# Performance work log

Measured on AMD Instinct MI355X. Metric: run time of the kernel, lower is better.

Reference implementation:

```python
import jax, jax.numpy as jnp
import numpy as np

N_NODES = 100000
N_EDGES = 1600000
D = 128
NUM_GRAPHS = 128


def setup_inputs() -> dict:
    key = jax.random.key(0)
    ks = jax.random.split(key, 9)
    s = 1.0 / np.sqrt(D)
    return {
        "h": jax.random.normal(ks[0], (N_NODES, D), dtype=jnp.float32),
        "W1_self": jax.random.normal(ks[1], (D, D), dtype=jnp.float32) * s,
        "W1_neigh": jax.random.normal(ks[2], (D, D), dtype=jnp.float32) * s,
        "b1": jnp.zeros((D,), dtype=jnp.float32),
        "W2_self": jax.random.normal(ks[3], (D, D), dtype=jnp.float32) * s,
        "W2_neigh": jax.random.normal(ks[4], (D, D), dtype=jnp.float32) * s,
        "b2": jnp.zeros((D,), dtype=jnp.float32),
        "src": jax.random.randint(ks[5], (N_EDGES,), 0, N_NODES, dtype=jnp.int32),
        "dst": jax.random.randint(ks[6], (N_EDGES,), 0, N_NODES, dtype=jnp.int32),
        "graph_ids": jnp.sort(jax.random.randint(ks[7], (N_NODES,), 0, NUM_GRAPHS, dtype=jnp.int32)),
    }


def _sage_conv(h, src, dst, W_self, W_neigh, b, deg_inv):
    # mean-aggregate in-neighbor features: gather src feats, segment-sum by dst
    agg = jax.ops.segment_sum(h[src], dst, num_segments=h.shape[0])  # [N, D]
    h_neigh = agg * deg_inv[:, None]
    return h @ W_self + h_neigh @ W_neigh + b


def reference(h, W1_self, W1_neigh, b1, W2_self, W2_neigh, b2, src, dst, graph_ids):
    N = h.shape[0]
    deg = jax.ops.segment_sum(jnp.ones_like(dst, dtype=h.dtype), dst, num_segments=N)
    deg_inv = jnp.where(deg > 0, 1.0 / jnp.maximum(deg, 1.0), 0.0)
    h1 = jax.nn.relu(_sage_conv(h, src, dst, W1_self, W1_neigh, b1, deg_inv))
    h2 = jax.nn.relu(_sage_conv(h1, src, dst, W2_self, W2_neigh, b2, deg_inv))
    # dgl.mean_nodes: per-graph mean of node features
    gsum = jax.ops.segment_sum(h2, graph_ids, num_segments=NUM_GRAPHS)  # [G, D]
    gcnt = jax.ops.segment_sum(jnp.ones((N,), dtype=h.dtype), graph_ids, num_segments=NUM_GRAPHS)
    return gsum / jnp.maximum(gcnt, 1.0)[:, None]
```

## Files before the change

kernel.cpp:

```cpp
#include <hip/hip_runtime.h>

#define N_NODES   100000
#define N_EDGES   1600000
#define D         128
#define NUM_GRAPHS 128

#define NB          196
#define BUCKET_NODES 512
#define BUCKET_CAP  10240
#define EPB         8192

#define N_TILES32   3125
#define GEMM_BLOCKS 782

typedef __attribute__((ext_vector_type(8)))  short bf16x8;
typedef __attribute__((ext_vector_type(8)))  unsigned short u16x8;
typedef __attribute__((ext_vector_type(2)))  unsigned int u32x2;
typedef __attribute__((ext_vector_type(4)))  unsigned int u32x4;
typedef __attribute__((ext_vector_type(16))) float f32x16;

__device__ __forceinline__ unsigned short f2bf(float f) {
    unsigned int u = __float_as_uint(f);
    u = (u + 0x7FFFu + ((u >> 16) & 1u)) >> 16;
    return (unsigned short)u;
}

__device__ __forceinline__ void acc_f8(float* acc, u32x2 v) {
    auto a0 = __builtin_amdgcn_cvt_pk_f32_fp8((int)v[0], false);
    auto a1 = __builtin_amdgcn_cvt_pk_f32_fp8((int)v[0], true);
    auto a2 = __builtin_amdgcn_cvt_pk_f32_fp8((int)v[1], false);
    auto a3 = __builtin_amdgcn_cvt_pk_f32_fp8((int)v[1], true);
    acc[0] += a0[0]; acc[1] += a0[1]; acc[2] += a1[0]; acc[3] += a1[1];
    acc[4] += a2[0]; acc[5] += a2[1]; acc[6] += a3[0]; acc[7] += a3[1];
}

__device__ __forceinline__ bf16x8 f8_to_bf16x8(u32x2 v) {
    auto f0 = __builtin_amdgcn_cvt_pk_f32_fp8((int)v[0], false);
    auto f1 = __builtin_amdgcn_cvt_pk_f32_fp8((int)v[0], true);
    auto f2 = __builtin_amdgcn_cvt_pk_f32_fp8((int)v[1], false);
    auto f3 = __builtin_amdgcn_cvt_pk_f32_fp8((int)v[1], true);
    u32x4 w;
    w[0] = __builtin_amdgcn_perm(__float_as_uint(f0[1]), __float_as_uint(f0[0]), 0x07060302u);
    w[1] = __builtin_amdgcn_perm(__float_as_uint(f1[1]), __float_as_uint(f1[0]), 0x07060302u);
    w[2] = __builtin_amdgcn_perm(__float_as_uint(f2[1]), __float_as_uint(f2[0]), 0x07060302u);
    w[3] = __builtin_amdgcn_perm(__float_as_uint(f3[1]), __float_as_uint(f3[0]), 0x07060302u);
    return *(bf16x8*)&w;
}

__global__ void k_misc(u32x4* __restrict__ zp, int n16,
                       const int* __restrict__ gid, int* __restrict__ gcnt,
                       const float* __restrict__ W1s, const float* __restrict__ W1n,
                       unsigned short* __restrict__ Wt1,
                       const float* __restrict__ W2s, const float* __restrict__ W2n,
                       unsigned short* __restrict__ Wt2,
                       const float* __restrict__ h, unsigned char* __restrict__ h8) {
    const int b = blockIdx.x;
    if (b < 17) {
        int i = b * 256 + threadIdx.x;
        if (i < n16) zp[i] = (u32x4){0u, 0u, 0u, 0u};
    } else if (b == 17) {
        int g = threadIdx.x;
        if (g >= NUM_GRAPHS) return;
        int lo = 0, hi = N_NODES;
        while (lo < hi) { int mid = (lo + hi) >> 1; if (gid[mid] < g) lo = mid + 1; else hi = mid; }
        int beg = lo;
        hi = N_NODES;
        while (lo < hi) { int mid = (lo + hi) >> 1; if (gid[mid] < g + 1) lo = mid + 1; else hi = mid; }
        gcnt[g] = lo - beg;
    } else if (b < 146) {
        int idx = (b - 18) * 256 + threadIdx.x;
        int j  = idx & 7;
        int l  = (idx >> 3) & 63;
        int fs = idx >> 9;
        int ct = fs >> 4, kt = fs & 15;
        int n  = ct * 32 + (l & 31);
        int k  = kt * 16 + 8 * (l >> 5) + j;
        float v = (k < 128) ? W1s[k * D + n] : W1n[(k - 128) * D + n];
        Wt1[idx] = f2bf(v);
    } else if (b < 274) {
        int idx = (b - 146) * 256 + threadIdx.x;
        int j  = idx & 7;
        int l  = (idx >> 3) & 63;
        int fs = idx >> 9;
        int ct = fs >> 4, kt = fs & 15;
        int n  = ct * 32 + (l & 31);
        int k  = kt * 16 + 8 * (l >> 5) + j;
        int p  = k & 127;
        int c  = 32 * (p & 3) + (p >> 2);
        float v = (k < 128) ? W2s[c * D + n] : W2n[c * D + n];
        Wt2[idx] = f2bf(v);
    } else {
        int i = (b - 274) * 256 + threadIdx.x;
        if (i >= N_NODES * (D / 8)) return;
        const float4* hv = (const float4*)h;
        float4 x = hv[2 * i], y = hv[2 * i + 1];
        int lo = __builtin_amdgcn_cvt_pk_fp8_f32(x.x, x.y, 0, false);
        lo = __builtin_amdgcn_cvt_pk_fp8_f32(x.z, x.w, lo, true);
        int hi = __builtin_amdgcn_cvt_pk_fp8_f32(y.x, y.y, 0, false);
        hi = __builtin_amdgcn_cvt_pk_fp8_f32(y.z, y.w, hi, true);
        u32x2 q; q[0] = (unsigned int)lo; q[1] = (unsigned int)hi;
        *(u32x2*)(h8 + (size_t)i * 8) = q;
    }
}

__global__ __launch_bounds__(256) void k_binplace(const int* __restrict__ src,
                                                  const int* __restrict__ dst,
                                                  int* __restrict__ gcur,
                                                  unsigned int* __restrict__ binned) {
    __shared__ unsigned int stag[EPB];
    __shared__ unsigned char sbk[EPB];
    __shared__ int hist[NB], lstart[NB], lcur[NB], gclaim[NB];
    __shared__ int scan[256];
    const int t = threadIdx.x;
    const int e0 = blockIdx.x * EPB;

    if (t < NB) hist[t] = 0;
    __syncthreads();

    int pk[32]; int bk[32];
#pragma unroll
    for (int i = 0; i < 32; ++i) {
        int e = e0 + t + 256 * i;
        if (e < N_EDGES) {
            int s = src[e], d = dst[e];
            bk[i] = d >> 9;
            pk[i] = (s << 9) | (d & 511);
            atomicAdd(&hist[bk[i]], 1);
        } else {
            bk[i] = -1; pk[i] = 0;
        }
    }
    __syncthreads();

    int hv = (t < NB) ? hist[t] : 0;
    scan[t] = hv;
    __syncthreads();
    for (int off = 1; off < 256; off <<= 1) {
        int add = (t >= off) ? scan[t - off] : 0;
        __syncthreads();
        scan[t] += add;
        __syncthreads();
    }
    if (t < NB) {
        int ex = scan[t] - hv;
        lstart[t] = ex;
        lcur[t]   = ex;
        gclaim[t] = atomicAdd(&gcur[t], hv);
    }
    __syncthreads();

#pragma unroll
    for (int i = 0; i < 32; ++i) {
        if (bk[i] >= 0) {
            int p = atomicAdd(&lcur[bk[i]], 1);
            stag[p] = (unsigned int)pk[i];
            sbk[p] = (unsigned char)bk[i];
        }
    }
    __syncthreads();

    const int total = scan[NB - 1];
    for (int j = t; j < total; j += 256) {
        int b = sbk[j];
        binned[(size_t)b * BUCKET_CAP + gclaim[b] + (j - lstart[b])] = stag[j];
    }
}

__global__ __launch_bounds__(256) void k_fill2(const unsigned int* __restrict__ binned,
                                               const int* __restrict__ gcur,
                                               int* __restrict__ adj,
                                               int* __restrict__ row_start,
                                               int* __restrict__ row_len) {
    __shared__ int hist[BUCKET_NODES], lstart[BUCKET_NODES], lcur[BUCKET_NODES];
    __shared__ int s2[256];
    const int t = threadIdx.x;
    const int b = blockIdx.x;
    const int C = gcur[b];
    const unsigned int* bp = binned + (size_t)b * BUCKET_CAP;

    hist[t] = 0; hist[t + 256] = 0;
    __syncthreads();
    for (int j = t; j < C; j += 256)
        atomicAdd(&hist[bp[j] & 511], 1);
    __syncthreads();

    int h0 = hist[2 * t], h1 = hist[2 * t + 1];
    int sv = h0 + h1;
    s2[t] = sv;
    __syncthreads();
    for (int off = 1; off < 256; off <<= 1) {
        int add = (t >= off) ? s2[t - off] : 0;
        __syncthreads();
        s2[t] += add;
        __syncthreads();
    }
    int ex = s2[t] - sv;
    lstart[2 * t] = ex;          lcur[2 * t] = ex;
    lstart[2 * t + 1] = ex + h0; lcur[2 * t + 1] = ex + h0;
    __syncthreads();

    for (int dl = t; dl < BUCKET_NODES; dl += 256) {
        int n = b * BUCKET_NODES + dl;
        if (n < N_NODES) {
            row_start[n] = b * BUCKET_CAP + lstart[dl];
            row_len[n]   = hist[dl];
        }
    }

    for (int j = t; j < C; j += 256) {
        unsigned int v = bp[j];
        int dl = v & 511;
        int pos = atomicAdd(&lcur[dl], 1);
        adj[(size_t)b * BUCKET_CAP + pos] = (int)(v >> 9);
    }
}

__global__ __launch_bounds__(256) void k_agg_f8(const unsigned char* __restrict__ hin,
                                                const int* __restrict__ row_start,
                                                const int* __restrict__ row_len,
                                                const int* __restrict__ adj,
                                                unsigned char* __restrict__ hout) {
    int node = blockIdx.x * 16 + (threadIdx.x >> 4);
    int sub = threadIdx.x & 15;
    if (node >= N_NODES) return;
    int beg = row_start[node];
    int len = row_len[node];
    int end = beg + len;
    const unsigned char* hsub = hin + sub * 8;
    float acc[8];
#pragma unroll
    for (int i = 0; i < 8; ++i) acc[i] = 0.f;
    int j = beg;
    for (; j + 7 < end; j += 8) {
        u32x2 v0 = *(const u32x2*)(hsub + (size_t)adj[j]     * D);
        u32x2 v1 = *(const u32x2*)(hsub + (size_t)adj[j + 1] * D);
        u32x2 v2 = *(const u32x2*)(hsub + (size_t)adj[j + 2] * D);
        u32x2 v3 = *(const u32x2*)(hsub + (size_t)adj[j + 3] * D);
        u32x2 v4 = *(const u32x2*)(hsub + (size_t)adj[j + 4] * D);
        u32x2 v5 = *(const u32x2*)(hsub + (size_t)adj[j + 5] * D);
        u32x2 v6 = *(const u32x2*)(hsub + (size_t)adj[j + 6] * D);
        u32x2 v7 = *(const u32x2*)(hsub + (size_t)adj[j + 7] * D);
        acc_f8(acc, v0); acc_f8(acc, v1); acc_f8(acc, v2); acc_f8(acc, v3);
        acc_f8(acc, v4); acc_f8(acc, v5); acc_f8(acc, v6); acc_f8(acc, v7);
    }
    for (; j + 3 < end; j += 4) {
        u32x2 v0 = *(const u32x2*)(hsub + (size_t)adj[j]     * D);
        u32x2 v1 = *(const u32x2*)(hsub + (size_t)adj[j + 1] * D);
        u32x2 v2 = *(const u32x2*)(hsub + (size_t)adj[j + 2] * D);
        u32x2 v3 = *(const u32x2*)(hsub + (size_t)adj[j + 3] * D);
        acc_f8(acc, v0); acc_f8(acc, v1); acc_f8(acc, v2); acc_f8(acc, v3);
    }
    for (; j < end; ++j) {
        u32x2 v0 = *(const u32x2*)(hsub + (size_t)adj[j] * D);
        acc_f8(acc, v0);
    }
    float inv = (len > 0) ? 1.f / (float)len : 0.f;
    int lo = __builtin_amdgcn_cvt_pk_fp8_f32(acc[0] * inv, acc[1] * inv, 0, false);
    lo = __builtin_amdgcn_cvt_pk_fp8_f32(acc[2] * inv, acc[3] * inv, lo, true);
    int hi = __builtin_amdgcn_cvt_pk_fp8_f32(acc[4] * inv, acc[5] * inv, 0, false);
    hi = __builtin_amdgcn_cvt_pk_fp8_f32(acc[6] * inv, acc[7] * inv, hi, true);
    u32x2 q; q[0] = (unsigned int)lo; q[1] = (unsigned int)hi;
    *(u32x2*)(hout + (size_t)node * D + sub * 8) = q;
}

template <int POOL>
__global__ __launch_bounds__(256) void k_gemm_mfma(
    const unsigned char* __restrict__ X0, const unsigned char* __restrict__ X1,
    const unsigned short* __restrict__ Wtp, const float* __restrict__ bias,
    unsigned char* __restrict__ outp8,
    const int* __restrict__ gid, float* __restrict__ gsum) {
    __shared__ unsigned short WS[D * 256];
    const int tid = threadIdx.x;
    const int wave = tid >> 6, lane = tid & 63;
    const int l31 = lane & 31, half = lane >> 5;
    const int gw = blockIdx.x * 4 + wave;
    const bool act = (gw < N_TILES32);

    bf16x8 a[16];
    if (act) {
        const int row = gw * 32 + l31;
        const unsigned char* x0 = X0 + (size_t)row * D + half * 8;
        const unsigned char* x1 = X1 + (size_t)row * D + half * 8;
        u32x2 v8[16];
#pragma unroll
        for (int kt = 0; kt < 8; ++kt)
            v8[kt] = *(const u32x2*)(x0 + kt * 16);
#pragma unroll
        for (int kt = 0; kt < 8; ++kt)
            v8[8 + kt] = *(const u32x2*)(x1 + kt * 16);
#pragma unroll
        for (int kt = 0; kt < 16; ++kt)
            a[kt] = f8_to_bf16x8(v8[kt]);
    }

    {
        const u16x8* g = (const u16x8*)Wtp;
        u16x8* s = (u16x8*)WS;
#pragma unroll
        for (int i = 0; i < 16; ++i) s[i * 256 + tid] = g[i * 256 + tid];
    }
    __syncthreads();
    if (!act) return;

    f32x16 acc[4];
#pragma unroll
    for (int ct = 0; ct < 4; ++ct)
#pragma unroll
        for (int i = 0; i < 16; ++i) acc[ct][i] = 0.f;

#pragma unroll
    for (int cp = 0; cp < 2; ++cp) {
        const int c0 = 2 * cp, c1 = 2 * cp + 1;
#pragma unroll
        for (int kt = 0; kt < 16; ++kt) {
            bf16x8 b0 = *(const bf16x8*)&WS[((c0 * 16 + kt) * 64 + lane) * 8];
            bf16x8 b1 = *(const bf16x8*)&WS[((c1 * 16 + kt) * 64 + lane) * 8];
            acc[c0] = __builtin_amdgcn_mfma_f32_32x32x16_bf16(a[kt], b0, acc[c0], 0, 0, 0);
            acc[c1] = __builtin_amdgcn_mfma_f32_32x32x16_bf16(a[kt], b1, acc[c1], 0, 0, 0);
        }
    }

    const int trow0 = gw * 32;
    float bia[4];
#pragma unroll
    for (int ct = 0; ct < 4; ++ct) bia[ct] = bias[ct * 32 + l31];

    if (POOL == 0) {
#pragma unroll
        for (int r = 0; r < 16; ++r) {
            int row = trow0 + (r & 3) + 8 * (r >> 2) + 4 * half;
            float f[4];
#pragma unroll
            for (int ct = 0; ct < 4; ++ct)
                f[ct] = fmaxf(acc[ct][r] + bia[ct], 0.f);
            int p8 = __builtin_amdgcn_cvt_pk_fp8_f32(f[0], f[1], 0, false);
            p8 = __builtin_amdgcn_cvt_pk_fp8_f32(f[2], f[3], p8, true);
            *(unsigned int*)(outp8 + (size_t)row * D + l31 * 4) = (unsigned int)p8;
        }
    } else {
        int g[16];
#pragma unroll
        for (int r = 0; r < 16; ++r)
            g[r] = gid[trow0 + (r & 3) + 8 * (r >> 2) + 4 * half];
#pragma unroll
        for (int ct = 0; ct < 4; ++ct) {
            int c = ct * 32 + l31;
            float run = 0.f; int curg = -1;
#pragma unroll
            for (int r = 0; r < 16; ++r) {
                float v = fmaxf(acc[ct][r] + bia[ct], 0.f);
                if (g[r] != curg) {
                    if (curg >= 0) atomicAdd(&gsum[curg * D + c], run);
                    curg = g[r]; run = v;
                } else {
                    run += v;
                }
            }
            if (curg >= 0) atomicAdd(&gsum[curg * D + c], run);
        }
    }
}

__global__ void k_final(const float* __restrict__ gsum, const int* __restrict__ gcnt,
                        float* __restrict__ out) {
    int i = blockIdx.x * blockDim.x + threadIdx.x;
    if (i < NUM_GRAPHS * D) {
        int g = i >> 7;
        int c = gcnt[g];
        out[i] = gsum[i] / (float)(c > 0 ? c : 1);
    }
}

extern "C" void kernel_launch(void* const* d_in, const int* in_sizes, int n_in,
                              void* d_out, int out_size, void* d_ws, size_t ws_size,
                              hipStream_t stream) {
    const float* h   = (const float*)d_in[0];
    const float* W1s = (const float*)d_in[1];
    const float* W1n = (const float*)d_in[2];
    const float* b1  = (const float*)d_in[3];
    const float* W2s = (const float*)d_in[4];
    const float* W2n = (const float*)d_in[5];
    const float* b2  = (const float*)d_in[6];
    const int* src   = (const int*)d_in[7];
    const int* dst   = (const int*)d_in[8];
    const int* gids  = (const int*)d_in[9];
    float* out = (float*)d_out;
    char* ws = (char*)d_ws;

    size_t off = 0;
    auto alloc = [&](size_t bytes) {
        size_t o = off;
        off = (off + bytes + 255) & ~(size_t)255;
        return o;
    };
    size_t z0         = off;
    size_t gcur_off   = alloc((size_t)NB * 4);
    size_t gsum_off   = alloc((size_t)NUM_GRAPHS * D * 4);
    size_t zlen       = off - z0;
    size_t gcnt_off   = alloc((size_t)NUM_GRAPHS * 4);
    size_t rs_off     = alloc((size_t)N_NODES * 4);
    size_t rl_off     = alloc((size_t)N_NODES * 4);
    size_t bin_off    = alloc((size_t)NB * BUCKET_CAP * 4);
    size_t adj_off    = alloc((size_t)NB * BUCKET_CAP * 4);
    size_t hn_off     = alloc((size_t)N_NODES * D);
    size_t h8_off     = alloc((size_t)N_NODES * D);
    size_t h18_off    = alloc((size_t)N_NODES * D);
    size_t wt1_off    = alloc((size_t)D * 256 * 2);
    size_t wt2_off    = alloc((size_t)D * 256 * 2);
    (void)ws_size;

    int*   gcur      = (int*)(ws + gcur_off);
    int*   gcnt      = (int*)(ws + gcnt_off);
    float* gsum      = (float*)(ws + gsum_off);
    int*   row_start = (int*)(ws + rs_off);
    int*   row_len   = (int*)(ws + rl_off);
    unsigned int* binned = (unsigned int*)(ws + bin_off);
    int*   adj       = (int*)(ws + adj_off);
    unsigned char*  hn8  = (unsigned char*)(ws + hn_off);
    unsigned char*  h8   = (unsigned char*)(ws + h8_off);
    unsigned char*  h1p8 = (unsigned char*)(ws + h18_off);
    unsigned short* Wt1 = (unsigned short*)(ws + wt1_off);
    unsigned short* Wt2 = (unsigned short*)(ws + wt2_off);

    const int n16 = (int)(zlen / 16);

    k_misc<<<6524, 256, 0, stream>>>((u32x4*)(ws + z0), n16, gids, gcnt,
                                     W1s, W1n, Wt1, W2s, W2n, Wt2, h, h8);

    const int nbin_blocks = (N_EDGES + EPB - 1) / EPB;
    k_binplace<<<nbin_blocks, 256, 0, stream>>>(src, dst, gcur, binned);
    k_fill2<<<NB, 256, 0, stream>>>(binned, gcur, adj, row_start, row_len);

    const int agg_blocks = (N_NODES + 15) / 16;

    k_agg_f8<<<agg_blocks, 256, 0, stream>>>(h8, row_start, row_len, adj, hn8);
    k_gemm_mfma<0><<<GEMM_BLOCKS, 256, 0, stream>>>(h8, hn8, Wt1, b1, h1p8,
                                                    nullptr, nullptr);
    k_agg_f8<<<agg_blocks, 256, 0, stream>>>(h1p8, row_start, row_len, adj, hn8);
    k_gemm_mfma<1><<<GEMM_BLOCKS, 256, 0, stream>>>(h1p8, hn8, Wt2, b2, nullptr,
                                                    gids, gsum);

    k_final<<<(NUM_GRAPHS * D + 255) / 256, 256, 0, stream>>>(gsum, gcnt, out);
}
```

Before: 167.7 us.

## Process two row tiles per GEMM wave with prefetch; halve binning edges per block

The GEMM kernel now launches 512 blocks and has each wave handle up to two 32-row tiles. The second tile's activations are prefetched before the first tile's MFMA work, so the 64KB weight staging into shared memory is paid once per two tiles instead of once per tile. Separately, the edge-binning kernel processes 4096 edges per block instead of 8192, which doubles its block count for more parallelism and fewer registers per thread. The cost is extra register pressure in the GEMM from holding the prefetched second tile.

```diff
diff --git a/kernel.cpp b/kernel.cpp
--- a/kernel.cpp
+++ b/kernel.cpp
@@ -8,10 +8,11 @@
 #define NB          196
 #define BUCKET_NODES 512
 #define BUCKET_CAP  10240
-#define EPB         8192
+#define EPB         4096
 
 #define N_TILES32   3125
-#define GEMM_BLOCKS 782
+#define GEMM_BLOCKS 512
+#define GEMM_WAVES  2048
 
 typedef __attribute__((ext_vector_type(8)))  short bf16x8;
 typedef __attribute__((ext_vector_type(8)))  unsigned short u16x8;
@@ -117,9 +118,9 @@
     if (t < NB) hist[t] = 0;
     __syncthreads();
 
-    int pk[32]; int bk[32];
-#pragma unroll
-    for (int i = 0; i < 32; ++i) {
+    int pk[EPB / 256]; int bk[EPB / 256];
+#pragma unroll
+    for (int i = 0; i < EPB / 256; ++i) {
         int e = e0 + t + 256 * i;
         if (e < N_EDGES) {
             int s = src[e], d = dst[e];
@@ -150,7 +151,7 @@
     __syncthreads();
 
 #pragma unroll
-    for (int i = 0; i < 32; ++i) {
+    for (int i = 0; i < EPB / 256; ++i) {
         if (bk[i] >= 0) {
             int p = atomicAdd(&lcur[bk[i]], 1);
             stag[p] = (unsigned int)pk[i];
@@ -264,43 +265,14 @@
 }
 
 template <int POOL>
-__global__ __launch_bounds__(256) void k_gemm_mfma(
-    const unsigned char* __restrict__ X0, const unsigned char* __restrict__ X1,
-    const unsigned short* __restrict__ Wtp, const float* __restrict__ bias,
-    unsigned char* __restrict__ outp8,
+__device__ __forceinline__ void gemm_tile(
+    const u32x2 (&v8)[16], const unsigned short* WS, int gw,
+    int lane, int l31, int half,
+    const float* __restrict__ bias, unsigned char* __restrict__ outp8,
     const int* __restrict__ gid, float* __restrict__ gsum) {
-    __shared__ unsigned short WS[D * 256];
-    const int tid = threadIdx.x;
-    const int wave = tid >> 6, lane = tid & 63;
-    const int l31 = lane & 31, half = lane >> 5;
-    const int gw = blockIdx.x * 4 + wave;
-    const bool act = (gw < N_TILES32);
-
     bf16x8 a[16];
-    if (act) {
-        const int row = gw * 32 + l31;
-        const unsigned char* x0 = X0 + (size_t)row * D + half * 8;
-        const unsigned char* x1 = X1 + (size_t)row * D + half * 8;
-        u32x2 v8[16];
-#pragma unroll
-        for (int kt = 0; kt < 8; ++kt)
-            v8[kt] = *(const u32x2*)(x0 + kt * 16);
-#pragma unroll
-        for (int kt = 0; kt < 8; ++kt)
-            v8[8 + kt] = *(const u32x2*)(x1 + kt * 16);
-#pragma unroll
-        for (int kt = 0; kt < 16; ++kt)
-            a[kt] = f8_to_bf16x8(v8[kt]);
-    }
-
-    {
-        const u16x8* g = (const u16x8*)Wtp;
-        u16x8* s = (u16x8*)WS;
-#pragma unroll
-        for (int i = 0; i < 16; ++i) s[i * 256 + tid] = g[i * 256 + tid];
-    }
-    __syncthreads();
-    if (!act) return;
+#pragma unroll
+    for (int kt = 0; kt < 16; ++kt) a[kt] = f8_to_bf16x8(v8[kt]);
 
     f32x16 acc[4];
 #pragma unroll
@@ -359,6 +331,55 @@
             if (curg >= 0) atomicAdd(&gsum[curg * D + c], run);
         }
     }
+}
+
+template <int POOL>
+__global__ __launch_bounds__(256) void k_gemm_mfma(
+    const unsigned char* __restrict__ X0, const unsigned char* __restrict__ X1,
+    const unsigned short* __restrict__ Wtp, const float* __restrict__ bias,
+    unsigned char* __restrict__ outp8,
+    const int* __restrict__ gid, float* __restrict__ gsum) {
+    __shared__ unsigned short WS[D * 256];
+    const int tid = threadIdx.x;
+    const int wave = tid >> 6, lane = tid & 63;
+    const int l31 = lane & 31, half = lane >> 5;
+    const int gw0 = blockIdx.x * 4 + wave;
+    const int gw1 = gw0 + GEMM_WAVES;
+    const bool has2 = (gw1 < N_TILES32);
+
+    u32x2 va[16];
+    {
+        const int row = gw0 * 32 + l31;
+        const unsigned char* x0 = X0 + (size_t)row * D + half * 8;
+        const unsigned char* x1 = X1 + (size_t)row * D + half * 8;
+#pragma unroll
+        for (int kt = 0; kt < 8; ++kt) va[kt] = *(const u32x2*)(x0 + kt * 16);
+#pragma unroll
+        for (int kt = 0; kt < 8; ++kt) va[8 + kt] = *(const u32x2*)(x1 + kt * 16);
+    }
+
+    {
+        const u16x8* g = (const u16x8*)Wtp;
+        u16x8* s = (u16x8*)WS;
+#pragma unroll
+        for (int i = 0; i < 16; ++i) s[i * 256 + tid] = g[i * 256 + tid];
+    }
+    __syncthreads();
+
+    u32x2 vb[16];
+    if (has2) {
+        const int row = gw1 * 32 + l31;
+        const unsigned char* x0 = X0 + (size_t)row * D + half * 8;
+        const unsigned char* x1 = X1 + (size_t)row * D + half * 8;
+#pragma unroll
+        for (int kt = 0; kt < 8; ++kt) vb[kt] = *(const u32x2*)(x0 + kt * 16);
+#pragma unroll
+        for (int kt = 0; kt < 8; ++kt) vb[8 + kt] = *(const u32x2*)(x1 + kt * 16);
+    }
+
+    gemm_tile<POOL>(va, WS, gw0, lane, l31, half, bias, outp8, gid, gsum);
+    if (has2)
+        gemm_tile<POOL>(vb, WS, gw1, lane, l31, half, bias, outp8, gid, gsum);
 }
 
 __global__ void k_final(const float* __restrict__ gsum, const int* __restrict__ gcnt,
```

After: 170.3 us. No clear change (+1.5%).
